# Performance work log

Measured on AMD Instinct MI355X. Metric: run time of the kernel, lower is better.

## Reference

```python
import jax, jax.numpy as jnp
import numpy as np

MIMO_RANK = 4  # module constant; q/k are identical across rank and mimo_v=mimo_out=ones,
               # q_bias=k_bias=0, so the rank sum equals MIMO_RANK * single-rank output.


def _rotary(t, ang):
    # split-half rotary: t [..., d], ang [..., d//2]
    d2 = t.shape[-1] // 2
    t1, t2 = t[..., :d2], t[..., d2:]
    c, s = jnp.cos(ang), jnp.sin(ang)
    return jnp.concatenate([t1 * c - t2 * s, t1 * s + t2 * c], axis=-1)


def setup_inputs() -> dict:
    key = jax.random.key(0)
    ks = jax.random.split(key, 6)
    b, l, h, dv, g, dqk = 2, 4096, 32, 64, 1, 128
    x = jax.random.normal(ks[0], (b, l, h, dv), jnp.float32)
    # positive step sizes (discretization dt)
    dt = jax.random.uniform(ks[1], (b, l, h), jnp.float32) * 0.05 + 1e-3
    # negative decay rates so exp(A*dt) < 1
    A = -(jax.random.uniform(ks[2], (h,), jnp.float32) + 0.5)
    B_gate = jax.random.normal(ks[3], (b, l, g, dqk), jnp.float32)
    C_gate = jax.random.normal(ks[4], (b, l, g, dqk), jnp.float32)
    D = jax.random.normal(ks[5], (h,), jnp.float32)
    return {"x": x, "dt": dt, "A": A, "B_gate": B_gate, "C_gate": C_gate,
            "D": D, "chunk_size": 64}


def reference(x, dt, A, B_gate, C_gate, D, chunk_size):
    # Mamba3 MIMO chunked selective scan (SSD) with rotary QK decay.
    # Recurrence per (b, h):  H_t = exp(A_h*dt_t) * H_{t-1} + rot(k_t) (dt_t x_t)^T
    #                         y_t = rot(q_t)^T H_t * MIMO_RANK + D_h * x_t
    # where q=C_gate, k=B_gate (shared across heads, ngroups=1) and the rotary
    # angle is theta_t = cumsum(dt) (TILELANG_ROTARY_DIV=2 -> dqk//2 angles).
    b, l, h, dv = x.shape
    dqk = C_gate.shape[-1]
    c = chunk_size
    n = l // c

    ang = jnp.cumsum(dt, axis=1)[..., None]                     # [b,l,h,1]
    ang = jnp.broadcast_to(ang, (b, l, h, dqk // 2))
    q = jnp.broadcast_to(C_gate[:, :, 0, :][:, :, None, :], (b, l, h, dqk))
    k = jnp.broadcast_to(B_gate[:, :, 0, :][:, :, None, :], (b, l, h, dqk))
    rotq = _rotary(q, ang)                                      # [b,l,h,dqk]
    rotk = _rotary(k, ang)
    adt = A[None, None, :] * dt                                 # [b,l,h] log-decay

    chunk = lambda t: t.reshape(b, n, c, *t.shape[2:])
    rq, rk = chunk(rotq), chunk(rotk)                           # [b,n,c,h,dqk]
    u = chunk(dt[..., None] * x)                                # [b,n,c,h,dv]
    a = chunk(adt)                                              # [b,n,c,h]
    cum = jnp.cumsum(a, axis=2)                                 # within-chunk cum log-decay

    # ---- intra-chunk (quadratic within chunk) ----
    seg = cum[:, :, :, None, :] - cum[:, :, None, :, :]         # [b,n,t,s,h]
    mask = jnp.tril(jnp.ones((c, c), bool))
    L = jnp.where(mask[None, None, :, :, None], jnp.exp(seg), 0.0)
    S = jnp.einsum('bnthd,bnshd->bntsh', rq, rk)                # [b,n,t,s,h]
    y_intra = jnp.einsum('bntsh,bnshe->bnthe', S * L, u)        # [b,n,c,h,dv]

    # ---- inter-chunk state recurrence ----
    decay_to_end = jnp.exp(cum[:, :, -1:, :] - cum)             # [b,n,c,h]
    dH = jnp.einsum('bnshd,bnsh,bnshe->bnhde', rk, decay_to_end, u)  # [b,n,h,dqk,dv]
    cdecay = jnp.exp(cum[:, :, -1, :])                          # [b,n,h] full-chunk decay

    def step(H, inp):
        dc, dh = inp
        Hprev = H
        return dc[:, :, None, None] * H + dh, Hprev

    H0 = jnp.zeros((b, h, dqk, dv), x.dtype)
    _, Hprev = jax.lax.scan(step, H0,
                            (jnp.moveaxis(cdecay, 1, 0), jnp.moveaxis(dH, 1, 0)))
    Hprev = jnp.moveaxis(Hprev, 0, 1)                           # [b,n,h,dqk,dv]

    y_inter = jnp.einsum('bnthd,bnth,bnhde->bnthe', rq, jnp.exp(cum), Hprev)

    y = MIMO_RANK * (y_intra + y_inter).reshape(b, l, h, dv)
    return y + D[None, None, :, None] * x
```

## Files before the change

kernel.cpp:

```cpp
#include <hip/hip_runtime.h>
#include <hip/hip_bf16.h>

#define BB 2
#define LL 4096
#define HH 32
#define DV 64
#define DQK 128
#define CC 64
#define NN 64
#define MIMO_RANK 4.0f

typedef __attribute__((ext_vector_type(8))) short short8;
typedef __attribute__((ext_vector_type(4))) float f32x4;

__device__ __forceinline__ ushort f2bf(float f) {
    __hip_bfloat16 h = __float2bfloat16(f);
    return *reinterpret_cast<ushort*>(&h);
}
__device__ __forceinline__ float bfbits2f(uint lo16) {
    return __uint_as_float(lo16 << 16);
}
__device__ __forceinline__ uint pkbf2(float lo, float hi) {
    return (uint)f2bf(lo) | ((uint)f2bf(hi) << 16);
}
union U8 { uint u[4]; short8 s; };

__device__ __forceinline__ int rk_off(int s, int d) {
    return s * 128 + (((((d >> 3) & 15) ^ (s & 7)) << 3)) + (d & 7);
}
__device__ __forceinline__ int uwT_off(int e, int s) {
    return e * 64 + ((((s >> 3) ^ (e & 7)) & 7) << 3) + (s & 7);
}
__device__ __forceinline__ int fSL(int t) {
    return (((t & 3) << 1) ^ ((t >> 2) & 7)) & 7;
}
__device__ __forceinline__ int SL_off(int t, int s) {
    return t * 64 + ((((s >> 3) ^ fSL(t)) & 7) << 3) + (s & 7);
}

__device__ __forceinline__ void make_rot_frags(const float* __restrict__ G,
                                               size_t gb, float cv, float sv,
                                               int kgrp, short8* fr) {
    #pragma unroll
    for (int kk = 0; kk < 4; ++kk) {
        int d0 = kk * 32 + kgrp;
        int dl = d0 & 63;
        bool low = d0 < 64;
        float4 a1 = *(const float4*)(G + gb + dl);
        float4 b1 = *(const float4*)(G + gb + dl + 4);
        float4 a2 = *(const float4*)(G + gb + dl + 64);
        float4 b2 = *(const float4*)(G + gb + dl + 68);
        float v0, v1, v2, v3, v4, v5, v6, v7;
        if (low) {
            v0 = a1.x * cv - a2.x * sv; v1 = a1.y * cv - a2.y * sv;
            v2 = a1.z * cv - a2.z * sv; v3 = a1.w * cv - a2.w * sv;
            v4 = b1.x * cv - b2.x * sv; v5 = b1.y * cv - b2.y * sv;
            v6 = b1.z * cv - b2.z * sv; v7 = b1.w * cv - b2.w * sv;
        } else {
            v0 = a1.x * sv + a2.x * cv; v1 = a1.y * sv + a2.y * cv;
            v2 = a1.z * sv + a2.z * cv; v3 = a1.w * sv + a2.w * cv;
            v4 = b1.x * sv + b2.x * cv; v5 = b1.y * sv + b2.y * cv;
            v6 = b1.z * sv + b2.z * cv; v7 = b1.w * sv + b2.w * cv;
        }
        U8 r;
        r.u[0] = pkbf2(v0, v1); r.u[1] = pkbf2(v2, v3);
        r.u[2] = pkbf2(v4, v5); r.u[3] = pkbf2(v6, v7);
        fr[kk] = r.s;
    }
}

__global__ __launch_bounds__(256) void k_scan_dt(const float* __restrict__ dt,
                                                 const float* __restrict__ A,
                                                 float4* __restrict__ tbl,
                                                 float* __restrict__ cdecay) {
    int bh = blockIdx.x;
    int b = bh / HH, h = bh % HH;
    int tid = threadIdx.x;
    const int PT = LL / 256;
    float v[PT];
    float s = 0.f;
    int tbase = tid * PT;
    for (int i = 0; i < PT; ++i) {
        v[i] = dt[(((size_t)b * LL + tbase + i) * HH) + h];
        s += v[i];
    }
    int lane = tid & 63, wv = tid >> 6;
    float ps = s;
    for (int off = 1; off < 64; off <<= 1) {
        float o = __shfl_up(ps, off, 64);
        if (lane >= off) ps += o;
    }
    __shared__ float wsum[4];
    if (lane == 63) wsum[wv] = ps;
    __syncthreads();
    float wadd = 0.f;
    for (int w = 0; w < wv; ++w) wadd += wsum[w];
    float run0 = wadd + ps - s;
    float run_end = run0 + s;
    float aend  = __shfl(run_end, lane | 3, 64);
    float aprev = __shfl(run0, lane & ~3, 64);
    float Ah = A[h];
    if ((tid & 3) == 0) {
        int n = tid >> 2;
        cdecay[(b * NN + n) * HH + h] = __expf(Ah * (aend - aprev));
    }
    float4* tb = tbl + ((size_t)(b * HH + h) * LL) + tbase;
    float run = run0;
    for (int i = 0; i < PT; ++i) {
        run += v[i];
        float sv, cv;
        __sincosf(run, &sv, &cv);
        float dw = __expf(Ah * (aend - run));
        float et = __expf(Ah * (run - aend));
        tb[i] = make_float4(cv, sv, v[i] * dw, et);
    }
}

__global__ __launch_bounds__(256, 3) void k_intra(
    const float* __restrict__ x, const float* __restrict__ Bg,
    const float* __restrict__ Cg, const float4* __restrict__ tbl,
    const float* __restrict__ Dd,
    ushort* __restrict__ ytmp, ushort* __restrict__ dH) {
    int n = blockIdx.x, h = blockIdx.y, b = blockIdx.z;
    int tid = threadIdx.x;
    int t0 = n * CC;

    __shared__ ushort rkS[CC * DQK];
    __shared__ ushort SLb[CC * CC];
    __shared__ ushort uwT[DV * CC];
    __shared__ float4 tblLds[CC];
    __shared__ float  xraw[CC * DV];

    int wv = tid >> 6, lane = tid & 63;
    int lrow = lane & 15;
    int g = lane >> 4;
    int kgrp = g * 8;
    int orow = g * 4;

    const float* BgRow = Bg + ((size_t)b * LL + t0) * DQK;
    const float4* tbg = tbl + ((size_t)(b * HH + h) * LL) + t0;

    float4 bg0[2], bg1[2], bg2[2], bg3[2], tvS[2];
    #pragma unroll
    for (int it = 0; it < 2; ++it) {
        int s = (tid >> 3) + 32 * it, oct = tid & 7;
        const float* p = BgRow + s * DQK + 8 * oct;
        bg0[it] = *(const float4*)(p);
        bg1[it] = *(const float4*)(p + 4);
        bg2[it] = *(const float4*)(p + 64);
        bg3[it] = *(const float4*)(p + 68);
        tvS[it] = tbg[s];
    }
    int t_own = 16 * wv + lrow;
    float4 tq = tbg[t_own];

    {
        const float4* tbsrc = tbg + lane;
        __builtin_amdgcn_global_load_lds((const void*)tbsrc, (void*)tblLds,
                                         16, 0, 0);
    }
    #pragma unroll
    for (int i = 0; i < 4; ++i) {
        int row = 16 * wv + 4 * i + (lane >> 4);
        const float* xsrc = x + ((((size_t)b * LL + t0 + row) * HH) + h) * DV
                            + 4 * (lane & 15);
        __builtin_amdgcn_global_load_lds((const void*)xsrc,
                                         (void*)(xraw + (16 * wv + 4 * i) * DV),
                                         16, 0, 0);
    }
    __builtin_amdgcn_sched_barrier(0);

    #pragma unroll
    for (int it = 0; it < 2; ++it) {
        int s = (tid >> 3) + 32 * it, oct = tid & 7;
        float cv = tvS[it].x, sv = tvS[it].y;
        U8 lo, hi;
        lo.u[0] = pkbf2(bg0[it].x * cv - bg2[it].x * sv, bg0[it].y * cv - bg2[it].y * sv);
        lo.u[1] = pkbf2(bg0[it].z * cv - bg2[it].z * sv, bg0[it].w * cv - bg2[it].w * sv);
        lo.u[2] = pkbf2(bg1[it].x * cv - bg3[it].x * sv, bg1[it].y * cv - bg3[it].y * sv);
        lo.u[3] = pkbf2(bg1[it].z * cv - bg3[it].z * sv, bg1[it].w * cv - bg3[it].w * sv);
        hi.u[0] = pkbf2(bg0[it].x * sv + bg2[it].x * cv, bg0[it].y * sv + bg2[it].y * cv);
        hi.u[1] = pkbf2(bg0[it].z * sv + bg2[it].z * cv, bg0[it].w * sv + bg2[it].w * cv);
        hi.u[2] = pkbf2(bg1[it].x * sv + bg3[it].x * cv, bg1[it].y * sv + bg3[it].y * cv);
        hi.u[3] = pkbf2(bg1[it].z * sv + bg3[it].z * cv, bg1[it].w * sv + bg3[it].w * cv);
        *(short8*)&rkS[rk_off(s, 8 * oct)] = lo.s;
        *(short8*)&rkS[rk_off(s, 8 * oct + 64)] = hi.s;
    }

    short8 aq[4];
    make_rot_frags(Cg, ((size_t)b * LL + t0 + t_own) * DQK, tq.x, tq.y, kgrp, aq);

    asm volatile("s_waitcnt vmcnt(0)" ::: "memory");
    __builtin_amdgcn_sched_barrier(0);
    #pragma unroll
    for (int it = 0; it < 2; ++it) {
        int s0 = 16 * wv + 8 * it;
        int e = lane;
        U8 pk;
        #pragma unroll
        for (int jp = 0; jp < 4; ++jp) {
            int sa = s0 + 2 * jp, sb = sa + 1;
            float xa = xraw[sa * DV + e] * tblLds[sa].z;
            float xb = xraw[sb * DV + e] * tblLds[sb].z;
            pk.u[jp] = pkbf2(xa, xb);
        }
        *(short8*)&uwT[uwT_off(e, s0)] = pk.s;
    }

    __syncthreads();

    f32x4 accS[4] = {{0.f,0.f,0.f,0.f},{0.f,0.f,0.f,0.f},
                     {0.f,0.f,0.f,0.f},{0.f,0.f,0.f,0.f}};
    #pragma unroll
    for (int kk = 0; kk < 4; ++kk) {
        #pragma unroll
        for (int nt = 0; nt < 4; ++nt) {
            int s = 16 * nt + lrow;
            const short8 bfr = *(const short8*)&rkS[rk_off(s, 32 * kk + kgrp)];
            accS[nt] = __builtin_amdgcn_mfma_f32_16x16x32_bf16(
                aq[kk], bfr, accS[nt], 0, 0, 0);
        }
    }

    short8 aH[2][2];
    #pragma unroll
    for (int kk = 0; kk < 2; ++kk) {
        #pragma unroll
        for (int mt = 0; mt < 2; ++mt) {
            int d = 32 * wv + 16 * mt + lrow;
            uint vv[8];
            #pragma unroll
            for (int j = 0; j < 8; ++j)
                vv[j] = rkS[rk_off(32 * kk + kgrp + j, d)];
            U8 pk;
            pk.u[0] = vv[0] | (vv[1] << 16);
            pk.u[1] = vv[2] | (vv[3] << 16);
            pk.u[2] = vv[4] | (vv[5] << 16);
            pk.u[3] = vv[6] | (vv[7] << 16);
            aH[kk][mt] = pk.s;
        }
    }

    #pragma unroll
    for (int rr = 0; rr < 4; ++rr) {
        int t = 16 * wv + orow + rr;
        float etv = tblLds[t].w;
        #pragma unroll
        for (int nt = 0; nt < 4; ++nt) {
            int s = 16 * nt + lrow;
            float v = (t >= s) ? accS[nt][rr] * etv : 0.f;
            SLb[SL_off(t, s)] = f2bf(v);
        }
    }

    __syncthreads();

    {
        f32x4 accY[4] = {{0.f,0.f,0.f,0.f},{0.f,0.f,0.f,0.f},
                         {0.f,0.f,0.f,0.f},{0.f,0.f,0.f,0.f}};
        #pragma unroll
        for (int kk = 0; kk < 2; ++kk) {
            const short8 a = *(const short8*)&SLb[SL_off(16 * wv + lrow, 32 * kk + kgrp)];
            #pragma unroll
            for (int nt = 0; nt < 4; ++nt) {
                const short8 bfr = *(const short8*)&uwT[uwT_off(16 * nt + lrow, 32 * kk + kgrp)];
                accY[nt] = __builtin_amdgcn_mfma_f32_16x16x32_bf16(
                    a, bfr, accY[nt], 0, 0, 0);
            }
        }
        float Dh = Dd[h];
        float fin[4][4];
        #pragma unroll
        for (int nt = 0; nt < 4; ++nt) {
            int e = 16 * nt + lrow;
            #pragma unroll
            for (int rr = 0; rr < 4; ++rr) {
                int t = 16 * wv + orow + rr;
                fin[nt][rr] = MIMO_RANK * accY[nt][rr] + Dh * xraw[t * DV + e];
            }
        }
        ushort* ytp = ytmp + (((size_t)(b * NN + n) * HH) + h) * (CC * DV);
        #pragma unroll
        for (int q = 0; q < 2; ++q) {
            U8 st;
            st.u[0] = pkbf2(fin[2 * q][0], fin[2 * q][1]);
            st.u[1] = pkbf2(fin[2 * q][2], fin[2 * q][3]);
            st.u[2] = pkbf2(fin[2 * q + 1][0], fin[2 * q + 1][1]);
            st.u[3] = pkbf2(fin[2 * q + 1][2], fin[2 * q + 1][3]);
            *(short8*)(ytp + ((size_t)(wv * 2 + q) * 64 + lane) * 8) = st.s;
        }
    }

    {
        f32x4 accH[2][4] = {{{0.f,0.f,0.f,0.f},{0.f,0.f,0.f,0.f},
                             {0.f,0.f,0.f,0.f},{0.f,0.f,0.f,0.f}},
                            {{0.f,0.f,0.f,0.f},{0.f,0.f,0.f,0.f},
                             {0.f,0.f,0.f,0.f},{0.f,0.f,0.f,0.f}}};
        #pragma unroll
        for (int kk = 0; kk < 2; ++kk) {
            #pragma unroll
            for (int mt = 0; mt < 2; ++mt) {
                #pragma unroll
                for (int nt = 0; nt < 4; ++nt) {
                    const short8 bfr = *(const short8*)&uwT[uwT_off(16 * nt + lrow, 32 * kk + kgrp)];
                    accH[mt][nt] = __builtin_amdgcn_mfma_f32_16x16x32_bf16(
                        aH[kk][mt], bfr, accH[mt][nt], 0, 0, 0);
                }
            }
        }
        ushort* dHp = dH + (((size_t)(b * NN + n) * HH) + h) * (DQK * DV);
        #pragma unroll
        for (int q = 0; q < 4; ++q) {
            int mt = q >> 1, np = q & 1;
            U8 st;
            st.u[0] = pkbf2(accH[mt][2 * np][0], accH[mt][2 * np][1]);
            st.u[1] = pkbf2(accH[mt][2 * np][2], accH[mt][2 * np][3]);
            st.u[2] = pkbf2(accH[mt][2 * np + 1][0], accH[mt][2 * np + 1][1]);
            st.u[3] = pkbf2(accH[mt][2 * np + 1][2], accH[mt][2 * np + 1][3]);
            *(short8*)(dHp + ((size_t)(wv * 4 + q) * 64 + lane) * 8) = st.s;
        }
    }
}

__global__ __launch_bounds__(256) void k_scan_chunks(
    uint* __restrict__ dH, const float* __restrict__ cdecay) {
    uint f = blockIdx.x * 256 + threadIdx.x;
    int b = (int)(f >> 17);
    uint r = f & 0x1FFFF;
    int h = (int)((r >> 12) & 31);
    uint base = ((uint)b << 23) | r;
    const float* cd = cdecay + (size_t)b * NN * HH + h;
    float h0 = 0.f, h1 = 0.f;
    for (int n = 0; n < NN; ++n) {
        uint a = base + ((uint)n << 17);
        uint v = dH[a];
        float v0 = bfbits2f(v & 0xFFFF), v1 = bfbits2f(v >> 16);
        dH[a] = pkbf2(h0, h1);
        float c = cd[n * HH];
        h0 = c * h0 + v0;
        h1 = c * h1 + v1;
    }
}

__global__ __launch_bounds__(256, 4) void k_inter(
    const float* __restrict__ Cg, const float4* __restrict__ tbl,
    const float* __restrict__ cdecay, const ushort* __restrict__ Hprev,
    const ushort* __restrict__ ytmp, float* __restrict__ out) {
    int n = blockIdx.x, h = blockIdx.y, b = blockIdx.z;
    int tid = threadIdx.x;
    int t0 = n * CC;

    __shared__ __align__(16) uint Hp[16 * 260];

    const float4* tb = tbl + ((size_t)(b * HH + h) * LL) + t0;
    float cdec = cdecay[(b * NN + n) * HH + h];

    int wv = tid >> 6, lane = tid & 63;
    int lrow = lane & 15;
    int g2 = lane >> 4;
    int kgrp = g2 * 8;
    int orow = g2 * 4;

    const ushort* ytp = ytmp + (((size_t)(b * NN + n) * HH) + h) * (CC * DV);
    U8 y0, y1;
    y0.s = *(const short8*)(ytp + ((size_t)(wv * 2 + 0) * 64 + lane) * 8);
    y1.s = *(const short8*)(ytp + ((size_t)(wv * 2 + 1) * 64 + lane) * 8);

    const uint* Hsrc = (const uint*)(Hprev + (((size_t)(b * NN + n) * HH) + h) * (DQK * DV));
    #pragma unroll
    for (int it = 0; it < 4; ++it) {
        int p = tid + 256 * it;
        uint4 v = *(const uint4*)(Hsrc + (size_t)p * 4);
        int row = p >> 6, c = p & 63;
        uint4* Hrow = (uint4*)&Hp[row * 260];
        Hrow[c] = v;
    }

    int t_own = 16 * wv + lrow;
    float4 tq = tb[t_own];
    short8 aq[4];
    make_rot_frags(Cg, ((size_t)b * LL + t0 + t_own) * DQK, tq.x, tq.y, kgrp, aq);
    __syncthreads();

    f32x4 accI[4] = {{0.f,0.f,0.f,0.f},{0.f,0.f,0.f,0.f},
                     {0.f,0.f,0.f,0.f},{0.f,0.f,0.f,0.f}};
    int mt = g2 >> 1;
    int gp0 = 2 * (g2 & 1);
    #pragma unroll
    for (int kk = 0; kk < 4; ++kk) {
        #pragma unroll
        for (int nt = 0; nt < 4; ++nt) {
            int q = mt * 2 + (nt >> 1);
            int row = kk * 4 + q;
            int sb = (nt & 1) * 2;
            const uint2 u0 = *(const uint2*)&Hp[row * 260 + (16 * gp0 + lrow) * 4 + sb];
            const uint2 u1 = *(const uint2*)&Hp[row * 260 + (16 * (gp0 + 1) + lrow) * 4 + sb];
            U8 fr;
            fr.u[0] = u0.x; fr.u[1] = u0.y; fr.u[2] = u1.x; fr.u[3] = u1.y;
            accI[nt] = __builtin_amdgcn_mfma_f32_16x16x32_bf16(
                aq[kk], fr.s, accI[nt], 0, 0, 0);
        }
    }

    #pragma unroll
    for (int rr = 0; rr < 4; ++rr) {
        int t = 16 * wv + orow + rr;
        float g4 = MIMO_RANK * tb[t].w * cdec;
        #pragma unroll
        for (int nt = 0; nt < 4; ++nt) {
            int e = 16 * nt + lrow;
            uint bits = (nt < 2) ? y0.u[(nt & 1) * 2 + (rr >> 1)]
                                 : y1.u[(nt & 1) * 2 + (rr >> 1)];
            float yv = bfbits2f((rr & 1) ? (bits >> 16) : (bits & 0xFFFF));
            size_t oidx = ((((size_t)b * LL + t0 + t) * HH) + h) * DV + e;
            out[oidx] = yv + g4 * accI[nt][rr];
        }
    }
}

extern "C" void kernel_launch(void* const* d_in, const int* in_sizes, int n_in,
                              void* d_out, int out_size, void* d_ws,
                              size_t ws_size, hipStream_t stream) {
    (void)in_sizes; (void)n_in; (void)out_size; (void)ws_size;
    const float* x  = (const float*)d_in[0];
    const float* dt = (const float*)d_in[1];
    const float* A  = (const float*)d_in[2];
    const float* Bg = (const float*)d_in[3];
    const float* Cg = (const float*)d_in[4];
    const float* Dd = (const float*)d_in[5];
    float* out = (float*)d_out;
    float* ws  = (float*)d_ws;

    float4* tbl    = (float4*)ws;
    float*  cdecay = ws + (size_t)BB * HH * LL * 4;
    ushort* dH     = (ushort*)(cdecay + BB * NN * HH);
    ushort* ytmp   = dH + (size_t)BB * NN * HH * DQK * DV;

    k_scan_dt<<<BB * HH, 256, 0, stream>>>(dt, A, tbl, cdecay);
    k_intra<<<dim3(NN, HH, BB), 256, 0, stream>>>(x, Bg, Cg, tbl, Dd, ytmp, dH);
    k_scan_chunks<<<(BB * HH * DQK * DV / 2) / 256, 256, 0, stream>>>(
        (uint*)dH, cdecay);
    k_inter<<<dim3(NN, HH, BB), 256, 0, stream>>>(Cg, tbl, cdecay, dH, ytmp, out);
}
```

Measured before the change: 100.4 us.

## Process two chunks per k_intra block and prefetch second chunk's B_gate into registers

```diff
diff --git a/kernel.cpp b/kernel.cpp
--- a/kernel.cpp
+++ b/kernel.cpp
@@ -69,6 +69,118 @@
     }
 }
 
+__device__ __forceinline__ void chunk_compute(
+    ushort* __restrict__ rkS, ushort* __restrict__ SLb,
+    ushort* __restrict__ uwT, const float4* __restrict__ tbc,
+    const float* __restrict__ xraw, const short8* aq,
+    int wv, int lane, int lrow, int kgrp, int orow, float Dh,
+    ushort* __restrict__ ytp, ushort* __restrict__ dHp) {
+    f32x4 accS[4] = {{0.f,0.f,0.f,0.f},{0.f,0.f,0.f,0.f},
+                     {0.f,0.f,0.f,0.f},{0.f,0.f,0.f,0.f}};
+    #pragma unroll
+    for (int kk = 0; kk < 4; ++kk) {
+        #pragma unroll
+        for (int nt = 0; nt < 4; ++nt) {
+            int s = 16 * nt + lrow;
+            const short8 bfr = *(const short8*)&rkS[rk_off(s, 32 * kk + kgrp)];
+            accS[nt] = __builtin_amdgcn_mfma_f32_16x16x32_bf16(
+                aq[kk], bfr, accS[nt], 0, 0, 0);
+        }
+    }
+    short8 aH[2][2];
+    #pragma unroll
+    for (int kk = 0; kk < 2; ++kk) {
+        #pragma unroll
+        for (int mt = 0; mt < 2; ++mt) {
+            int d = 32 * wv + 16 * mt + lrow;
+            uint vv[8];
+            #pragma unroll
+            for (int j = 0; j < 8; ++j)
+                vv[j] = rkS[rk_off(32 * kk + kgrp + j, d)];
+            U8 pk;
+            pk.u[0] = vv[0] | (vv[1] << 16);
+            pk.u[1] = vv[2] | (vv[3] << 16);
+            pk.u[2] = vv[4] | (vv[5] << 16);
+            pk.u[3] = vv[6] | (vv[7] << 16);
+            aH[kk][mt] = pk.s;
+        }
+    }
+    #pragma unroll
+    for (int rr = 0; rr < 4; ++rr) {
+        int t = 16 * wv + orow + rr;
+        float etv = tbc[t].w;
+        #pragma unroll
+        for (int nt = 0; nt < 4; ++nt) {
+            int s = 16 * nt + lrow;
+            float v = (t >= s) ? accS[nt][rr] * etv : 0.f;
+            SLb[SL_off(t, s)] = f2bf(v);
+        }
+    }
+    __syncthreads();
+
+    {
+        f32x4 accY[4] = {{0.f,0.f,0.f,0.f},{0.f,0.f,0.f,0.f},
+                         {0.f,0.f,0.f,0.f},{0.f,0.f,0.f,0.f}};
+        #pragma unroll
+        for (int kk = 0; kk < 2; ++kk) {
+            const short8 a = *(const short8*)&SLb[SL_off(16 * wv + lrow, 32 * kk + kgrp)];
+            #pragma unroll
+            for (int nt = 0; nt < 4; ++nt) {
+                const short8 bfr = *(const short8*)&uwT[uwT_off(16 * nt + lrow, 32 * kk + kgrp)];
+                accY[nt] = __builtin_amdgcn_mfma_f32_16x16x32_bf16(
+                    a, bfr, accY[nt], 0, 0, 0);
+            }
+        }
+        float fin[4][4];
+        #pragma unroll
+        for (int nt = 0; nt < 4; ++nt) {
+            int e = 16 * nt + lrow;
+            #pragma unroll
+            for (int rr = 0; rr < 4; ++rr) {
+                int t = 16 * wv + orow + rr;
+                fin[nt][rr] = MIMO_RANK * accY[nt][rr] + Dh * xraw[t * DV + e];
+            }
+        }
+        #pragma unroll
+        for (int q = 0; q < 2; ++q) {
+            U8 st;
+            st.u[0] = pkbf2(fin[2 * q][0], fin[2 * q][1]);
+            st.u[1] = pkbf2(fin[2 * q][2], fin[2 * q][3]);
+            st.u[2] = pkbf2(fin[2 * q + 1][0], fin[2 * q + 1][1]);
+            st.u[3] = pkbf2(fin[2 * q + 1][2], fin[2 * q + 1][3]);
+            *(short8*)(ytp + ((size_t)(wv * 2 + q) * 64 + lane) * 8) = st.s;
+        }
+    }
+    {
+        f32x4 accH[2][4] = {{{0.f,0.f,0.f,0.f},{0.f,0.f,0.f,0.f},
+                             {0.f,0.f,0.f,0.f},{0.f,0.f,0.f,0.f}},
+                            {{0.f,0.f,0.f,0.f},{0.f,0.f,0.f,0.f},
+                             {0.f,0.f,0.f,0.f},{0.f,0.f,0.f,0.f}}};
+        #pragma unroll
+        for (int kk = 0; kk < 2; ++kk) {
+            #pragma unroll
+            for (int mt = 0; mt < 2; ++mt) {
+                #pragma unroll
+                for (int nt = 0; nt < 4; ++nt) {
+                    const short8 bfr = *(const short8*)&uwT[uwT_off(16 * nt + lrow, 32 * kk + kgrp)];
+                    accH[mt][nt] = __builtin_amdgcn_mfma_f32_16x16x32_bf16(
+                        aH[kk][mt], bfr, accH[mt][nt], 0, 0, 0);
+                }
+            }
+        }
+        #pragma unroll
+        for (int q = 0; q < 4; ++q) {
+            int mt = q >> 1, np = q & 1;
+            U8 st;
+            st.u[0] = pkbf2(accH[mt][2 * np][0], accH[mt][2 * np][1]);
+            st.u[1] = pkbf2(accH[mt][2 * np][2], accH[mt][2 * np][3]);
+            st.u[2] = pkbf2(accH[mt][2 * np + 1][0], accH[mt][2 * np + 1][1]);
+            st.u[3] = pkbf2(accH[mt][2 * np + 1][2], accH[mt][2 * np + 1][3]);
+            *(short8*)(dHp + ((size_t)(wv * 4 + q) * 64 + lane) * 8) = st.s;
+        }
+    }
+}
+
 __global__ __launch_bounds__(256) void k_scan_dt(const float* __restrict__ dt,
                                                  const float* __restrict__ A,
                                                  float4* __restrict__ tbl,
@@ -121,14 +233,15 @@
     const float* __restrict__ Cg, const float4* __restrict__ tbl,
     const float* __restrict__ Dd,
     ushort* __restrict__ ytmp, ushort* __restrict__ dH) {
-    int n = blockIdx.x, h = blockIdx.y, b = blockIdx.z;
+    int np_ = blockIdx.x, h = blockIdx.y, b = blockIdx.z;
     int tid = threadIdx.x;
-    int t0 = n * CC;
+    int nA = 2 * np_, nB = nA + 1;
+    int t0A = nA * CC, t0B = nB * CC;
 
     __shared__ ushort rkS[CC * DQK];
     __shared__ ushort SLb[CC * CC];
     __shared__ ushort uwT[DV * CC];
-    __shared__ float4 tblLds[CC];
+    __shared__ float4 tblLds[2][CC];
     __shared__ float  xraw[CC * DV];
 
     int wv = tid >> 6, lane = tid & 63;
@@ -136,33 +249,33 @@
     int g = lane >> 4;
     int kgrp = g * 8;
     int orow = g * 4;
-
-    const float* BgRow = Bg + ((size_t)b * LL + t0) * DQK;
-    const float4* tbg = tbl + ((size_t)(b * HH + h) * LL) + t0;
-
-    float4 bg0[2], bg1[2], bg2[2], bg3[2], tvS[2];
+    float Dh = Dd[h];
+
+    const float* BgRowA = Bg + ((size_t)b * LL + t0A) * DQK;
+    const float* BgRowB = Bg + ((size_t)b * LL + t0B) * DQK;
+    const float4* tbgA = tbl + ((size_t)(b * HH + h) * LL) + t0A;
+    const float4* tbgB = tbgA + CC;
+
+    float4 bgA0[2], bgA1[2], bgA2[2], bgA3[2], tvSA[2];
     #pragma unroll
     for (int it = 0; it < 2; ++it) {
         int s = (tid >> 3) + 32 * it, oct = tid & 7;
-        const float* p = BgRow + s * DQK + 8 * oct;
-        bg0[it] = *(const float4*)(p);
-        bg1[it] = *(const float4*)(p + 4);
-        bg2[it] = *(const float4*)(p + 64);
-        bg3[it] = *(const float4*)(p + 68);
-        tvS[it] = tbg[s];
+        const float* p = BgRowA + s * DQK + 8 * oct;
+        bgA0[it] = *(const float4*)(p);
+        bgA1[it] = *(const float4*)(p + 4);
+        bgA2[it] = *(const float4*)(p + 64);
+        bgA3[it] = *(const float4*)(p + 68);
+        tvSA[it] = tbgA[s];
     }
     int t_own = 16 * wv + lrow;
-    float4 tq = tbg[t_own];
-
-    {
-        const float4* tbsrc = tbg + lane;
-        __builtin_amdgcn_global_load_lds((const void*)tbsrc, (void*)tblLds,
-                                         16, 0, 0);
-    }
+    float4 tqA = tbgA[t_own];
+
+    __builtin_amdgcn_global_load_lds((const void*)(tbgA + lane),
+                                     (void*)tblLds[0], 16, 0, 0);
     #pragma unroll
     for (int i = 0; i < 4; ++i) {
         int row = 16 * wv + 4 * i + (lane >> 4);
-        const float* xsrc = x + ((((size_t)b * LL + t0 + row) * HH) + h) * DV
+        const float* xsrc = x + ((((size_t)b * LL + t0A + row) * HH) + h) * DV
                             + 4 * (lane & 15);
         __builtin_amdgcn_global_load_lds((const void*)xsrc,
                                          (void*)(xraw + (16 * wv + 4 * i) * DV),
@@ -173,22 +286,22 @@
     #pragma unroll
     for (int it = 0; it < 2; ++it) {
         int s = (tid >> 3) + 32 * it, oct = tid & 7;
-        float cv = tvS[it].x, sv = tvS[it].y;
+        float cv = tvSA[it].x, sv = tvSA[it].y;
         U8 lo, hi;
-        lo.u[0] = pkbf2(bg0[it].x * cv - bg2[it].x * sv, bg0[it].y * cv - bg2[it].y * sv);
-        lo.u[1] = pkbf2(bg0[it].z * cv - bg2[it].z * sv, bg0[it].w * cv - bg2[it].w * sv);
-        lo.u[2] = pkbf2(bg1[it].x * cv - bg3[it].x * sv, bg1[it].y * cv - bg3[it].y * sv);
-        lo.u[3] = pkbf2(bg1[it].z * cv - bg3[it].z * sv, bg1[it].w * cv - bg3[it].w * sv);
-        hi.u[0] = pkbf2(bg0[it].x * sv + bg2[it].x * cv, bg0[it].y * sv + bg2[it].y * cv);
-        hi.u[1] = pkbf2(bg0[it].z * sv + bg2[it].z * cv, bg0[it].w * sv + bg2[it].w * cv);
-        hi.u[2] = pkbf2(bg1[it].x * sv + bg3[it].x * cv, bg1[it].y * sv + bg3[it].y * cv);
-        hi.u[3] = pkbf2(bg1[it].z * sv + bg3[it].z * cv, bg1[it].w * sv + bg3[it].w * cv);
+        lo.u[0] = pkbf2(bgA0[it].x * cv - bgA2[it].x * sv, bgA0[it].y * cv - bgA2[it].y * sv);
+        lo.u[1] = pkbf2(bgA0[it].z * cv - bgA2[it].z * sv, bgA0[it].w * cv - bgA2[it].w * sv);
+        lo.u[2] = pkbf2(bgA1[it].x * cv - bgA3[it].x * sv, bgA1[it].y * cv - bgA3[it].y * sv);
+        lo.u[3] = pkbf2(bgA1[it].z * cv - bgA3[it].z * sv, bgA1[it].w * cv - bgA3[it].w * sv);
+        hi.u[0] = pkbf2(bgA0[it].x * sv + bgA2[it].x * cv, bgA0[it].y * sv + bgA2[it].y * cv);
+        hi.u[1] = pkbf2(bgA0[it].z * sv + bgA2[it].z * cv, bgA0[it].w * sv + bgA2[it].w * cv);
+        hi.u[2] = pkbf2(bgA1[it].x * sv + bgA3[it].x * cv, bgA1[it].y * sv + bgA3[it].y * cv);
+        hi.u[3] = pkbf2(bgA1[it].z * sv + bgA3[it].z * cv, bgA1[it].w * sv + bgA3[it].w * cv);
         *(short8*)&rkS[rk_off(s, 8 * oct)] = lo.s;
         *(short8*)&rkS[rk_off(s, 8 * oct + 64)] = hi.s;
     }
 
-    short8 aq[4];
-    make_rot_frags(Cg, ((size_t)b * LL + t0 + t_own) * DQK, tq.x, tq.y, kgrp, aq);
+    short8 aqA[4];
+    make_rot_frags(Cg, ((size_t)b * LL + t0A + t_own) * DQK, tqA.x, tqA.y, kgrp, aqA);
 
     asm volatile("s_waitcnt vmcnt(0)" ::: "memory");
     __builtin_amdgcn_sched_barrier(0);
@@ -200,126 +313,92 @@
         #pragma unroll
         for (int jp = 0; jp < 4; ++jp) {
             int sa = s0 + 2 * jp, sb = sa + 1;
-            float xa = xraw[sa * DV + e] * tblLds[sa].z;
-            float xb = xraw[sb * DV + e] * tblLds[sb].z;
+            float xa = xraw[sa * DV + e] * tblLds[0][sa].z;
+            float xb = xraw[sb * DV + e] * tblLds[0][sb].z;
             pk.u[jp] = pkbf2(xa, xb);
         }
         *(short8*)&uwT[uwT_off(e, s0)] = pk.s;
     }
 
+    float4 bgB0[2], bgB1[2], bgB2[2], bgB3[2], tvSB[2];
+    #pragma unroll
+    for (int it = 0; it < 2; ++it) {
+        int s = (tid >> 3) + 32 * it, oct = tid & 7;
+        const float* p = BgRowB + s * DQK + 8 * oct;
+        bgB0[it] = *(const float4*)(p);
+        bgB1[it] = *(const float4*)(p + 4);
+        bgB2[it] = *(const float4*)(p + 64);
+        bgB3[it] = *(const float4*)(p + 68);
+        tvSB[it] = tbgB[s];
+    }
+    float4 tqB = tbgB[t_own];
+    __builtin_amdgcn_sched_barrier(0);
+
     __syncthreads();
 
-    f32x4 accS[4] = {{0.f,0.f,0.f,0.f},{0.f,0.f,0.f,0.f},
-                     {0.f,0.f,0.f,0.f},{0.f,0.f,0.f,0.f}};
-    #pragma unroll
-    for (int kk = 0; kk < 4; ++kk) {
-        #pragma unroll
-        for (int nt = 0; nt < 4; ++nt) {
-            int s = 16 * nt + lrow;
-            const short8 bfr = *(const short8*)&rkS[rk_off(s, 32 * kk + kgrp)];
-            accS[nt] = __builtin_amdgcn_mfma_f32_16x16x32_bf16(
-                aq[kk], bfr, accS[nt], 0, 0, 0);
-        }
-    }
-
-    short8 aH[2][2];
-    #pragma unroll
-    for (int kk = 0; kk < 2; ++kk) {
-        #pragma unroll
-        for (int mt = 0; mt < 2; ++mt) {
-            int d = 32 * wv + 16 * mt + lrow;
-            uint vv[8];
-            #pragma unroll
-            for (int j = 0; j < 8; ++j)
-                vv[j] = rkS[rk_off(32 * kk + kgrp + j, d)];
-            U8 pk;
-            pk.u[0] = vv[0] | (vv[1] << 16);
-            pk.u[1] = vv[2] | (vv[3] << 16);
-            pk.u[2] = vv[4] | (vv[5] << 16);
-            pk.u[3] = vv[6] | (vv[7] << 16);
-            aH[kk][mt] = pk.s;
-        }
-    }
-
-    #pragma unroll
-    for (int rr = 0; rr < 4; ++rr) {
-        int t = 16 * wv + orow + rr;
-        float etv = tblLds[t].w;
-        #pragma unroll
-        for (int nt = 0; nt < 4; ++nt) {
-            int s = 16 * nt + lrow;
-            float v = (t >= s) ? accS[nt][rr] * etv : 0.f;
-            SLb[SL_off(t, s)] = f2bf(v);
-        }
-    }
+    chunk_compute(rkS, SLb, uwT, tblLds[0], xraw, aqA, wv, lane, lrow, kgrp,
+                  orow, Dh,
+                  ytmp + (((size_t)(b * NN + nA) * HH) + h) * (CC * DV),
+                  dH + (((size_t)(b * NN + nA) * HH) + h) * (DQK * DV));
 
     __syncthreads();
 
-    {
-        f32x4 accY[4] = {{0.f,0.f,0.f,0.f},{0.f,0.f,0.f,0.f},
-                         {0.f,0.f,0.f,0.f},{0.f,0.f,0.f,0.f}};
-        #pragma unroll
-        for (int kk = 0; kk < 2; ++kk) {
-            const short8 a = *(const short8*)&SLb[SL_off(16 * wv + lrow, 32 * kk + kgrp)];
-            #pragma unroll
-            for (int nt = 0; nt < 4; ++nt) {
-                const short8 bfr = *(const short8*)&uwT[uwT_off(16 * nt + lrow, 32 * kk + kgrp)];
-                accY[nt] = __builtin_amdgcn_mfma_f32_16x16x32_bf16(
-                    a, bfr, accY[nt], 0, 0, 0);
-            }
-        }
-        float Dh = Dd[h];
-        float fin[4][4];
-        #pragma unroll
-        for (int nt = 0; nt < 4; ++nt) {
-            int e = 16 * nt + lrow;
-            #pragma unroll
-            for (int rr = 0; rr < 4; ++rr) {
-                int t = 16 * wv + orow + rr;
-                fin[nt][rr] = MIMO_RANK * accY[nt][rr] + Dh * xraw[t * DV + e];
-            }
-        }
-        ushort* ytp = ytmp + (((size_t)(b * NN + n) * HH) + h) * (CC * DV);
-        #pragma unroll
-        for (int q = 0; q < 2; ++q) {
-            U8 st;
-            st.u[0] = pkbf2(fin[2 * q][0], fin[2 * q][1]);
-            st.u[1] = pkbf2(fin[2 * q][2], fin[2 * q][3]);
-            st.u[2] = pkbf2(fin[2 * q + 1][0], fin[2 * q + 1][1]);
-            st.u[3] = pkbf2(fin[2 * q + 1][2], fin[2 * q + 1][3]);
-            *(short8*)(ytp + ((size_t)(wv * 2 + q) * 64 + lane) * 8) = st.s;
-        }
-    }
-
-    {
-        f32x4 accH[2][4] = {{{0.f,0.f,0.f,0.f},{0.f,0.f,0.f,0.f},
-                             {0.f,0.f,0.f,0.f},{0.f,0.f,0.f,0.f}},
-                            {{0.f,0.f,0.f,0.f},{0.f,0.f,0.f,0.f},
-                             {0.f,0.f,0.f,0.f},{0.f,0.f,0.f,0.f}}};
-        #pragma unroll
-        for (int kk = 0; kk < 2; ++kk) {
-            #pragma unroll
-            for (int mt = 0; mt < 2; ++mt) {
-                #pragma unroll
-                for (int nt = 0; nt < 4; ++nt) {
-                    const short8 bfr = *(const short8*)&uwT[uwT_off(16 * nt + lrow, 32 * kk + kgrp)];
-                    accH[mt][nt] = __builtin_amdgcn_mfma_f32_16x16x32_bf16(
-                        aH[kk][mt], bfr, accH[mt][nt], 0, 0, 0);
-                }
-            }
-        }
-        ushort* dHp = dH + (((size_t)(b * NN + n) * HH) + h) * (DQK * DV);
-        #pragma unroll
-        for (int q = 0; q < 4; ++q) {
-            int mt = q >> 1, np = q & 1;
-            U8 st;
-            st.u[0] = pkbf2(accH[mt][2 * np][0], accH[mt][2 * np][1]);
-            st.u[1] = pkbf2(accH[mt][2 * np][2], accH[mt][2 * np][3]);
-            st.u[2] = pkbf2(accH[mt][2 * np + 1][0], accH[mt][2 * np + 1][1]);
-            st.u[3] = pkbf2(accH[mt][2 * np + 1][2], accH[mt][2 * np + 1][3]);
-            *(short8*)(dHp + ((size_t)(wv * 4 + q) * 64 + lane) * 8) = st.s;
-        }
-    }
+    __builtin_amdgcn_global_load_lds((const void*)(tbgB + lane),
+                                     (void*)tblLds[1], 16, 0, 0);
+    #pragma unroll
+    for (int i = 0; i < 4; ++i) {
+        int row = 16 * wv + 4 * i + (lane >> 4);
+        const float* xsrc = x + ((((size_t)b * LL + t0B + row) * HH) + h) * DV
+                            + 4 * (lane & 15);
+        __builtin_amdgcn_global_load_lds((const void*)xsrc,
+                                         (void*)(xraw + (16 * wv + 4 * i) * DV),
+                                         16, 0, 0);
+    }
+    __builtin_amdgcn_sched_barrier(0);
+
+    #pragma unroll
+    for (int it = 0; it < 2; ++it) {
+        int s = (tid >> 3) + 32 * it, oct = tid & 7;
+        float cv = tvSB[it].x, sv = tvSB[it].y;
+        U8 lo, hi;
+        lo.u[0] = pkbf2(bgB0[it].x * cv - bgB2[it].x * sv, bgB0[it].y * cv - bgB2[it].y * sv);
+        lo.u[1] = pkbf2(bgB0[it].z * cv - bgB2[it].z * sv, bgB0[it].w * cv - bgB2[it].w * sv);
+        lo.u[2] = pkbf2(bgB1[it].x * cv - bgB3[it].x * sv, bgB1[it].y * cv - bgB3[it].y * sv);
+        lo.u[3] = pkbf2(bgB1[it].z * cv - bgB3[it].z * sv, bgB1[it].w * cv - bgB3[it].w * sv);
+        hi.u[0] = pkbf2(bgB0[it].x * sv + bgB2[it].x * cv, bgB0[it].y * sv + bgB2[it].y * cv);
+        hi.u[1] = pkbf2(bgB0[it].z * sv + bgB2[it].z * cv, bgB0[it].w * sv + bgB2[it].w * cv);
+        hi.u[2] = pkbf2(bgB1[it].x * sv + bgB3[it].x * cv, bgB1[it].y * sv + bgB3[it].y * cv);
+        hi.u[3] = pkbf2(bgB1[it].z * sv + bgB3[it].z * cv, bgB1[it].w * sv + bgB3[it].w * cv);
+        *(short8*)&rkS[rk_off(s, 8 * oct)] = lo.s;
+        *(short8*)&rkS[rk_off(s, 8 * oct + 64)] = hi.s;
+    }
+
+    short8 aqB[4];
+    make_rot_frags(Cg, ((size_t)b * LL + t0B + t_own) * DQK, tqB.x, tqB.y, kgrp, aqB);
+
+    asm volatile("s_waitcnt vmcnt(0)" ::: "memory");
+    __builtin_amdgcn_sched_barrier(0);
+    #pragma unroll
+    for (int it = 0; it < 2; ++it) {
+        int s0 = 16 * wv + 8 * it;
+        int e = lane;
+        U8 pk;
+        #pragma unroll
+        for (int jp = 0; jp < 4; ++jp) {
+            int sa = s0 + 2 * jp, sb = sa + 1;
+            float xa = xraw[sa * DV + e] * tblLds[1][sa].z;
+            float xb = xraw[sb * DV + e] * tblLds[1][sb].z;
+            pk.u[jp] = pkbf2(xa, xb);
+        }
+        *(short8*)&uwT[uwT_off(e, s0)] = pk.s;
+    }
+
+    __syncthreads();
+
+    chunk_compute(rkS, SLb, uwT, tblLds[1], xraw, aqB, wv, lane, lrow, kgrp,
+                  orow, Dh,
+                  ytmp + (((size_t)(b * NN + nB) * HH) + h) * (CC * DV),
+                  dH + (((size_t)(b * NN + nB) * HH) + h) * (DQK * DV));
 }
 
 __global__ __launch_bounds__(256) void k_scan_chunks(
@@ -437,7 +516,8 @@
     ushort* ytmp   = dH + (size_t)BB * NN * HH * DQK * DV;
 
     k_scan_dt<<<BB * HH, 256, 0, stream>>>(dt, A, tbl, cdecay);
-    k_intra<<<dim3(NN, HH, BB), 256, 0, stream>>>(x, Bg, Cg, tbl, Dd, ytmp, dH);
+    k_intra<<<dim3(NN / 2, HH, BB), 256, 0, stream>>>(x, Bg, Cg, tbl, Dd,
+                                                      ytmp, dH);
     k_scan_chunks<<<(BB * HH * DQK * DV / 2) / 256, 256, 0, stream>>>(
         (uint*)dH, cdecay);
     k_inter<<<dim3(NN, HH, BB), 256, 0, stream>>>(Cg, tbl, cdecay, dH, ytmp, out);
```

Result: slower. 115.2 us (+14.8%).
